# Kernel tuning notes

Measured on AMD Instinct MI355X. Metric: run time of the kernel, lower is better.

The kernel has to match this reference:

```python
import jax, jax.numpy as jnp
import numpy as np
from jax import lax

B, T, I = 256, 720, 16   # batch, seq_len, input_dim
H = 128                  # hidden_dim
PRED_LEN = 96


def lstm_cell(x, h, c, W_ih, W_hh, b):
    # PyTorch gate order: i, f, g, o ; b = b_ih + b_hh (combined)
    gates = x @ W_ih.T + h @ W_hh.T + b
    i, f, g, o = jnp.split(gates, 4, axis=-1)
    c = jax.nn.sigmoid(f) * c + jax.nn.sigmoid(i) * jnp.tanh(g)
    h = jax.nn.sigmoid(o) * jnp.tanh(c)
    return h, c


def setup_inputs() -> dict:
    key = jax.random.key(0)
    ks = jax.random.split(key, 16)
    k = 1.0 / np.sqrt(H)
    u = lambda kk, shape: jax.random.uniform(kk, shape, jnp.float32, -k, k)
    inp = {
        "x": jax.random.normal(ks[0], (B, T, I), jnp.float32),
        # encoder (bidirectional, 1 layer): forward + backward directions
        "e_Wih_f": u(ks[1], (4 * H, I)), "e_Whh_f": u(ks[2], (4 * H, H)), "e_b_f": u(ks[3], (4 * H,)),
        "e_Wih_b": u(ks[4], (4 * H, I)), "e_Whh_b": u(ks[5], (4 * H, H)), "e_b_b": u(ks[6], (4 * H,)),
        # decoder (bidirectional, 1 layer)
        "d_Wih_f": u(ks[7], (4 * H, I)), "d_Whh_f": u(ks[8], (4 * H, H)), "d_b_f": u(ks[9], (4 * H,)),
        "d_Wih_b": u(ks[10], (4 * H, I)), "d_Whh_b": u(ks[11], (4 * H, H)), "d_b_b": u(ks[12], (4 * H,)),
        # final linear: (2H -> I)
        "W_lin": u(ks[13], (I, 2 * H)), "b_lin": u(ks[14], (I,)),
    }
    return inp


def reference(x, e_Wih_f, e_Whh_f, e_b_f, e_Wih_b, e_Whh_b, e_b_b,
              d_Wih_f, d_Whh_f, d_b_f, d_Wih_b, d_Whh_b, d_b_b,
              W_lin, b_lin):
    xt = jnp.transpose(x, (1, 0, 2))  # [T, B, I] time-major
    h0 = jnp.zeros((B, H), x.dtype)
    c0 = jnp.zeros((B, H), x.dtype)

    # ---- encoder: bidirectional LSTM; only final (h, c) per direction is used ----
    def enc_f(carry, xt_t):
        h, c = lstm_cell(xt_t, carry[0], carry[1], e_Wih_f, e_Whh_f, e_b_f)
        return (h, c), None

    def enc_b(carry, xt_t):
        h, c = lstm_cell(xt_t, carry[0], carry[1], e_Wih_b, e_Whh_b, e_b_b)
        return (h, c), None

    (hf, cf), _ = lax.scan(enc_f, (h0, c0), xt)
    (hb, cb), _ = lax.scan(enc_b, (h0, c0), xt[::-1])

    def dec_step(carry, _):
        inp, hf, cf, hb, cb = carry
        hf, cf = lstm_cell(inp, hf, cf, d_Wih_f, d_Whh_f, d_b_f)
        hb, cb = lstm_cell(inp, hb, cb, d_Wih_b, d_Whh_b, d_b_b)
        # seq_len==1 so out_f = forward hidden, out_b = backward hidden
        out = jnp.concatenate([hf, hb], axis=-1) @ W_lin.T + b_lin  # [B, I]
        return (out, hf, cf, hb, cb), out

    init = (x[:, -1, :], hf, cf, hb, cb)
    _, outs = lax.scan(dec_step, init, None, length=PRED_LEN)  # [P, B, I]
    return jnp.transpose(outs, (1, 0, 2))  # [B, pred_len, I]
```

## Files before the change

### kernel.cpp

```cpp
#include <hip/hip_runtime.h>
#include <math.h>

#define TB    720
#define NI    16
#define NH    128
#define NG    512
#define PRED  96
#define CHUNK 90

typedef _Float16 h2    __attribute__((ext_vector_type(2)));
typedef _Float16 f16x4 __attribute__((ext_vector_type(4)));
typedef _Float16 f16x8 __attribute__((ext_vector_type(8)));
typedef float    f32x4 __attribute__((ext_vector_type(4)));

#define LOG2E  1.4426950408889634f
#define LOG2E2 2.8853900817779268f

__device__ __forceinline__ float rcpf_(float v) {
#if __has_builtin(__builtin_amdgcn_rcpf)
    return __builtin_amdgcn_rcpf(v);
#else
    return 1.0f / v;
#endif
}
__device__ __forceinline__ float ex2(float v) {
#if __has_builtin(__builtin_amdgcn_exp2f)
    return __builtin_amdgcn_exp2f(v);
#else
    return exp2f(v);
#endif
}

__device__ __forceinline__ unsigned int packf16(float a, float b) {
    h2 p; p.x = (_Float16)a; p.y = (_Float16)b;
    return __builtin_bit_cast(unsigned int, p);
}
__device__ __forceinline__ f32x4 MFMA(f16x8 a, f16x8 b, f32x4 c) {
    return __builtin_amdgcn_mfma_f32_16x16x32_f16(a, b, c, 0, 0, 0);
}
__device__ __forceinline__ f16x8 mk8s(const float* p, float s) {
    f16x8 v;
    v[0] = (_Float16)(p[0]  * s); v[1] = (_Float16)(p[1]  * s);
    v[2] = (_Float16)(p[2]  * s); v[3] = (_Float16)(p[3]  * s);
    v[4] = (_Float16)(p[16] * s); v[5] = (_Float16)(p[17] * s);
    v[6] = (_Float16)(p[18] * s); v[7] = (_Float16)(p[19] * s);
    return v;
}
__device__ __forceinline__ int opaque(int v) { asm volatile("" : "+v"(v)); return v; }

#define CELLBODY(CV, CS, HWPTR, CWBV) { \
    float ei_ = ex2(-(CV)[0]), ef_ = ex2(-(CV)[1]); \
    float eg_ = ex2((CV)[2]),  eo_ = ex2(-(CV)[3]); \
    float di_ = 1.f + ei_, df_ = 1.f + ef_, dg_ = 1.f + eg_, dq_ = 1.f + eo_; \
    float r1_ = rcpf_(di_ * df_), r2_ = rcpf_(dq_ * dg_); \
    float si_ = r1_ * df_, sf_ = r1_ * di_, so_ = r2_ * dg_; \
    float tg_ = __builtin_fmaf(-2.f * r2_, dq_, 1.f); \
    (CS) = sf_ * (CS) + si_ * tg_; \
    float ec_ = ex2((CS) * LOG2E2); \
    float th_ = __builtin_fmaf(-2.f, rcpf_(1.f + ec_), 1.f); \
    float hv_ = so_ * th_; \
    *(_Float16*)((char*)(HWPTR) + (CWBV)) = (_Float16)hv_; }

__global__ __launch_bounds__(1024, 4)
void enc_kernel(const float* __restrict__ x,
                const float* __restrict__ Wih_f, const float* __restrict__ Whh_f, const float* __restrict__ b_f,
                const float* __restrict__ Wih_b, const float* __restrict__ Whh_b, const float* __restrict__ b_b,
                float* __restrict__ st)
{
    __shared__ _Float16 hbuf0[16 * NH];
    __shared__ _Float16 hbuf1[16 * NH];
    __shared__ unsigned int xsh[CHUNK * 128];

    const int blk = blockIdx.x;
    const int dir = blk & 1;
    const int b0  = (blk >> 1) << 4;
    const int t   = threadIdx.x;
    const int wv  = t >> 6;
    const int l   = t & 63;
    const int lr  = l & 15;
    const int lk  = l >> 4;

    const float* Wih = dir ? Wih_b : Wih_f;
    const float* Whh = dir ? Whh_b : Whh_f;
    const float* bv  = dir ? b_b   : b_f;

    const int mt0 = 2 * wv, mt1 = 2 * wv + 1;
    const int R0 = mt0 * 16 + lr, R1 = mt1 * 16 + lr;
    const int or0 = (R0 & 3) * 128 + (R0 >> 2);
    const int or1 = (R1 & 3) * 128 + (R1 >> 2);
    const float s0 = ((or0 >> 7) == 2) ? LOG2E2 : LOG2E;
    const float s1 = ((or1 >> 7) == 2) ? LOG2E2 : LOG2E;
    const float* p0 = Whh + (size_t)or0 * NH + lk * 4;
    const float* p1 = Whh + (size_t)or1 * NH + lk * 4;
    f16x8 w0_0 = mk8s(p0, s0), w0_1 = mk8s(p0 + 32, s0), w0_2 = mk8s(p0 + 64, s0), w0_3 = mk8s(p0 + 96, s0);
    f16x8 w1_0 = mk8s(p1, s1), w1_1 = mk8s(p1 + 32, s1), w1_2 = mk8s(p1 + 64, s1), w1_3 = mk8s(p1 + 96, s1);

    f16x8 ax0, ax1;
#define MKAXR(DST, OR, SC) { \
    const float* xr_ = Wih + (size_t)(OR) * NI + lk * 4; \
    DST[0] = (_Float16)(xr_[0] * (SC)); DST[1] = (_Float16)(xr_[1] * (SC)); \
    DST[2] = (_Float16)(xr_[2] * (SC)); DST[3] = (_Float16)(xr_[3] * (SC)); \
    DST[4] = (_Float16)(bv[(OR)] * (SC)); \
    DST[5] = (_Float16)0.f; DST[6] = (_Float16)0.f; DST[7] = (_Float16)0.f; }
    MKAXR(ax0, or0, s0) MKAXR(ax1, or1, s1)
#undef MKAXR

    const int d0 = mt0 * 4 + lk, d1 = mt1 * 4 + lk;

    ((unsigned int*)hbuf0)[t] = 0u;
    float cs0 = 0.f, cs1 = 0.f;

    const int hro0 = 0 * 1024 + lk * 256 + lr * 16;
    const int hro1 = 1 * 1024 + lk * 256 + lr * 16;
    const int hro2 = 2 * 1024 + lk * 256 + lr * 16;
    const int hro3 = 3 * 1024 + lk * 256 + lr * 16;
#define CWB(D) ((((D) >> 5) * 1024) + ((((D) & 15) >> 2) * 256) + lr * 16 + (((((D) & 31) >> 4) * 4 + ((D) & 3)) * 2))
    const int cwb0 = CWB(d0), cwb1 = CWB(d1);
#undef CWB
    const int xoff = lk * 128 + lr * 8;
    const unsigned int oneku = (lk == 0) ? 0x00003c00u : 0u;
    const f32x4 CZ = {0.f, 0.f, 0.f, 0.f};
    __syncthreads();

#define STEP(HR, HW, SI) { \
    const char* hrb_ = (const char*)(HR); \
    f16x8 bx; \
    { uint2 xq_ = *(const uint2*)((const char*)xsh + (SI) * 512 + xoff); \
      ((unsigned int*)&bx)[0] = xq_.x; ((unsigned int*)&bx)[1] = xq_.y; \
      ((unsigned int*)&bx)[2] = oneku; ((unsigned int*)&bx)[3] = 0u; } \
    f32x4 C0 = MFMA(ax0, bx, CZ); \
    f32x4 C1 = MFMA(ax1, bx, CZ); \
    f16x8 bh_; \
    bh_ = *(const f16x8*)(hrb_ + hro0); \
    C0 = MFMA(w0_0, bh_, C0); C1 = MFMA(w1_0, bh_, C1); \
    bh_ = *(const f16x8*)(hrb_ + hro1); \
    C0 = MFMA(w0_1, bh_, C0); C1 = MFMA(w1_1, bh_, C1); \
    bh_ = *(const f16x8*)(hrb_ + hro2); \
    C0 = MFMA(w0_2, bh_, C0); C1 = MFMA(w1_2, bh_, C1); \
    bh_ = *(const f16x8*)(hrb_ + hro3); \
    C0 = MFMA(w0_3, bh_, C0); C1 = MFMA(w1_3, bh_, C1); \
    CELLBODY(C0, cs0, HW, cwb0) \
    CELLBODY(C1, cs1, HW, cwb1) \
    __syncthreads(); }

    for (int c = 0; c < 8; ++c) {
        {
            const int c0 = c * CHUNK;
            for (int i = t; i < 16 * CHUNK * 8; i += 1024) {
                const int br  = i / (CHUNK * 8);
                const int rem = i - br * (CHUNK * 8);
                const int ti  = rem >> 3;
                const int dw  = rem & 7;
                const int s_  = c0 + ti;
                const int tt  = dir ? (TB - 1 - s_) : s_;
                float2 v = *(const float2*)(x + ((size_t)(b0 + br) * TB + tt) * NI + dw * 2);
                xsh[ti * 128 + (dw >> 1) * 32 + br * 2 + (dw & 1)] = packf16(v.x, v.y);
            }
        }
        __syncthreads();
        for (int si2 = 0; si2 < CHUNK / 2; ++si2) {
            STEP(hbuf0, hbuf1, si2 * 2)
            STEP(hbuf1, hbuf0, si2 * 2 + 1)
        }
    }
#undef STEP

    {
        const size_t base = ((size_t)(b0 + lr) * 2 + dir) * 2 * NH;
#define CWB(D) ((((D) >> 5) * 1024) + ((((D) & 15) >> 2) * 256) + lr * 16 + (((((D) & 31) >> 4) * 4 + ((D) & 3)) * 2))
        st[base + d0]      = (float)*(const _Float16*)((const char*)hbuf0 + CWB(d0));
        st[base + NH + d0] = cs0;
        st[base + d1]      = (float)*(const _Float16*)((const char*)hbuf0 + CWB(d1));
        st[base + NH + d1] = cs1;
#undef CWB
    }
}

__global__ __launch_bounds__(1024, 4)
void dec_kernel(const float* __restrict__ x,
                const float* __restrict__ Wih_f, const float* __restrict__ Whh_f, const float* __restrict__ b_f,
                const float* __restrict__ Wih_b, const float* __restrict__ Whh_b, const float* __restrict__ b_b,
                const float* __restrict__ Wlin, const float* __restrict__ blin,
                const float* __restrict__ st, float* __restrict__ out)
{
    __shared__ _Float16 hF0[16 * NH], hF1[16 * NH];
    __shared__ _Float16 hB0[16 * NH], hB1[16 * NH];
    __shared__ unsigned int wlin_s[8 * 64 * 4];
    __shared__ unsigned int inpH[16 * 8];
    __shared__ float obuf[PRED * 16 * 16];

    const int b0   = blockIdx.x << 4;
    const int t    = threadIdx.x;
    const int wv   = t >> 6;
    const int cell = wv >> 3;
    const int wvv  = wv & 7;
    const int l    = t & 63;
    const int lr   = l & 15;
    const int lk   = l >> 4;

    const float* Wih = cell ? Wih_b : Wih_f;
    const float* Whh = cell ? Whh_b : Whh_f;
    const float* bv  = cell ? b_b   : b_f;

    if (t < 512) {
        const int f = t >> 6, ll = t & 63;
        const int elr = ll & 15, elk = ll >> 4;
        const float* wr = Wlin + elr * 256 + f * 32 + elk * 4;
        uint4 q;
        q.x = packf16(wr[0],  wr[1]);  q.y = packf16(wr[2],  wr[3]);
        q.z = packf16(wr[16], wr[17]); q.w = packf16(wr[18], wr[19]);
        *(uint4*)&wlin_s[(f * 64 + ll) * 4] = q;
    }

    const int mt0 = 4 * wvv, mt1 = 4 * wvv + 1, mt2 = 4 * wvv + 2, mt3 = 4 * wvv + 3;
    const int R0 = mt0 * 16 + lr, R1 = mt1 * 16 + lr, R2 = mt2 * 16 + lr, R3 = mt3 * 16 + lr;
    const int or0 = (R0 & 3) * 128 + (R0 >> 2);
    const int or1 = (R1 & 3) * 128 + (R1 >> 2);
    const int or2 = (R2 & 3) * 128 + (R2 >> 2);
    const int or3 = (R3 & 3) * 128 + (R3 >> 2);
    const float s0 = ((or0 >> 7) == 2) ? LOG2E2 : LOG2E;
    const float s1 = ((or1 >> 7) == 2) ? LOG2E2 : LOG2E;
    const float s2 = ((or2 >> 7) == 2) ? LOG2E2 : LOG2E;
    const float s3 = ((or3 >> 7) == 2) ? LOG2E2 : LOG2E;
    const float* p0 = Whh + (size_t)or0 * NH + lk * 4;
    const float* p1 = Whh + (size_t)or1 * NH + lk * 4;
    const float* p2 = Whh + (size_t)or2 * NH + lk * 4;
    const float* p3 = Whh + (size_t)or3 * NH + lk * 4;
    f16x8 w0_0 = mk8s(p0, s0), w0_1 = mk8s(p0 + 32, s0), w0_2 = mk8s(p0 + 64, s0), w0_3 = mk8s(p0 + 96, s0);
    f16x8 w1_0 = mk8s(p1, s1), w1_1 = mk8s(p1 + 32, s1), w1_2 = mk8s(p1 + 64, s1), w1_3 = mk8s(p1 + 96, s1);
    f16x8 w2_0 = mk8s(p2, s2), w2_1 = mk8s(p2 + 32, s2), w2_2 = mk8s(p2 + 64, s2), w2_3 = mk8s(p2 + 96, s2);
    f16x8 w3_0 = mk8s(p3, s3), w3_1 = mk8s(p3 + 32, s3), w3_2 = mk8s(p3 + 64, s3), w3_3 = mk8s(p3 + 96, s3);

    f16x8 ax0, ax1, ax2, ax3;
#define MKAXR(DST, OR, SC) { \
    const float* xr_ = Wih + (size_t)(OR) * NI + lk * 4; \
    DST[0] = (_Float16)(xr_[0] * (SC)); DST[1] = (_Float16)(xr_[1] * (SC)); \
    DST[2] = (_Float16)(xr_[2] * (SC)); DST[3] = (_Float16)(xr_[3] * (SC)); \
    DST[4] = (_Float16)(bv[(OR)] * (SC)); \
    DST[5] = (_Float16)0.f; DST[6] = (_Float16)0.f; DST[7] = (_Float16)0.f; }
    MKAXR(ax0, or0, s0) MKAXR(ax1, or1, s1) MKAXR(ax2, or2, s2) MKAXR(ax3, or3, s3)
#undef MKAXR

    const int d0 = mt0 * 4 + lk, d1 = mt1 * 4 + lk, d2 = mt2 * 4 + lk, d3 = mt3 * 4 + lk;

    const int hro0 = 0 * 1024 + lk * 256 + lr * 16;
    const int hro1 = 1 * 1024 + lk * 256 + lr * 16;
    const int hro2 = 2 * 1024 + lk * 256 + lr * 16;
    const int hro3 = 3 * 1024 + lk * 256 + lr * 16;
#define CWB(D) ((((D) >> 5) * 1024) + ((((D) & 15) >> 2) * 256) + lr * 16 + (((((D) & 31) >> 4) * 4 + ((D) & 3)) * 2))
    const int cwb0 = CWB(d0), cwb1 = CWB(d1), cwb2 = CWB(d2), cwb3 = CWB(d3);
    float cs0, cs1, cs2, cs3;
    {
        _Float16* hini = cell ? hB0 : hF0;
        const size_t bs = ((size_t)(b0 + lr) * 2 + cell) * 2 * NH;
        *(_Float16*)((char*)hini + cwb0) = (_Float16)st[bs + d0];  cs0 = st[bs + NH + d0];
        *(_Float16*)((char*)hini + cwb1) = (_Float16)st[bs + d1];  cs1 = st[bs + NH + d1];
        *(_Float16*)((char*)hini + cwb2) = (_Float16)st[bs + d2];  cs2 = st[bs + NH + d2];
        *(_Float16*)((char*)hini + cwb3) = (_Float16)st[bs + d3];  cs3 = st[bs + NH + d3];
    }
#undef CWB
    if (t < 128) {
        const int ilr = t >> 3, idw = t & 7;
        const float2 v = *(const float2*)(x + ((size_t)(b0 + ilr) * TB + (TB - 1)) * NI + idw * 2);
        inpH[ilr * 8 + idw] = packf16(v.x, v.y);
    }
    const float bl0 = blin[4 * lk + 0], bl1 = blin[4 * lk + 1];
    const float bl2 = blin[4 * lk + 2], bl3 = blin[4 * lk + 3];
    const unsigned int oneku = (lk == 0) ? 0x00003c00u : 0u;
    const f32x4 CZ = {0.f, 0.f, 0.f, 0.f};
    __syncthreads();

#define STEPD(HRF, HWF, HRB, HWB, S) { \
    const char* hr_ = cell ? (const char*)(HRB) : (const char*)(HRF); \
    char*       hw_ = cell ? (char*)(HWB)       : (char*)(HWF); \
    f16x8 bx; \
    { uint2 xq_ = *(const uint2*)((const char*)inpH + lr * 32 + lk * 8); \
      ((unsigned int*)&bx)[0] = xq_.x; ((unsigned int*)&bx)[1] = xq_.y; \
      ((unsigned int*)&bx)[2] = oneku; ((unsigned int*)&bx)[3] = 0u; } \
    f32x4 C0 = MFMA(ax0, bx, CZ); f32x4 C1 = MFMA(ax1, bx, CZ); \
    f32x4 C2 = MFMA(ax2, bx, CZ); f32x4 C3 = MFMA(ax3, bx, CZ); \
    f16x8 bh_; \
    bh_ = *(const f16x8*)(hr_ + hro0); \
    C0 = MFMA(w0_0, bh_, C0); C1 = MFMA(w1_0, bh_, C1); \
    C2 = MFMA(w2_0, bh_, C2); C3 = MFMA(w3_0, bh_, C3); \
    bh_ = *(const f16x8*)(hr_ + hro1); \
    C0 = MFMA(w0_1, bh_, C0); C1 = MFMA(w1_1, bh_, C1); \
    C2 = MFMA(w2_1, bh_, C2); C3 = MFMA(w3_1, bh_, C3); \
    bh_ = *(const f16x8*)(hr_ + hro2); \
    C0 = MFMA(w0_2, bh_, C0); C1 = MFMA(w1_2, bh_, C1); \
    C2 = MFMA(w2_2, bh_, C2); C3 = MFMA(w3_2, bh_, C3); \
    bh_ = *(const f16x8*)(hr_ + hro3); \
    C0 = MFMA(w0_3, bh_, C0); C1 = MFMA(w1_3, bh_, C1); \
    C2 = MFMA(w2_3, bh_, C2); C3 = MFMA(w3_3, bh_, C3); \
    CELLBODY(C0, cs0, hw_, cwb0) \
    CELLBODY(C1, cs1, hw_, cwb1) \
    CELLBODY(C2, cs2, hw_, cwb2) \
    CELLBODY(C3, cs3, hw_, cwb3) \
    __syncthreads(); \
    if (wv == 0) { \
        f32x4 P = CZ; \
        f16x8 af_, bf_; \
        _Pragma("unroll") \
        for (int f = 0; f < 8; ++f) { \
            af_ = *(const f16x8*)((const char*)wlin_s + opaque((f * 64 + l) * 16)); \
            const char* hb_ = (f < 4) ? (const char*)(HWF) + f * 1024 \
                                      : (const char*)(HWB) + (f - 4) * 1024; \
            bf_ = *(const f16x8*)(hb_ + lk * 256 + lr * 16); \
            P = MFMA(af_, bf_, P); \
        } \
        float o0 = P[0] + bl0, o1 = P[1] + bl1, o2 = P[2] + bl2, o3 = P[3] + bl3; \
        float* ob_ = obuf + (S) * 256 + (4 * lk) * 16 + lr; \
        ob_[0] = o0; ob_[16] = o1; ob_[32] = o2; ob_[48] = o3; \
        inpH[lr * 8 + lk * 2]     = packf16(o0, o1); \
        inpH[lr * 8 + lk * 2 + 1] = packf16(o2, o3); \
    } \
    __syncthreads(); }

    for (int s2 = 0; s2 < PRED / 2; ++s2) {
        STEPD(hF0, hF1, hB0, hB1, s2 * 2)
        STEPD(hF1, hF0, hB1, hB0, s2 * 2 + 1)
    }
#undef STEPD

    for (int i = t; i < PRED * 256; i += 1024) {
        const int lr2 = i / (PRED * NI);
        const int rem = i - lr2 * (PRED * NI);
        const int s   = rem >> 4;
        const int j   = rem & 15;
        out[(size_t)(b0 + lr2) * PRED * NI + rem] = obuf[s * 256 + j * 16 + lr2];
    }
}

extern "C" void kernel_launch(void* const* d_in, const int* in_sizes, int n_in,
                              void* d_out, int out_size, void* d_ws, size_t ws_size,
                              hipStream_t stream)
{
    const float* x      = (const float*)d_in[0];
    const float* eWih_f = (const float*)d_in[1];
    const float* eWhh_f = (const float*)d_in[2];
    const float* eb_f   = (const float*)d_in[3];
    const float* eWih_b = (const float*)d_in[4];
    const float* eWhh_b = (const float*)d_in[5];
    const float* eb_b   = (const float*)d_in[6];
    const float* dWih_f = (const float*)d_in[7];
    const float* dWhh_f = (const float*)d_in[8];
    const float* db_f   = (const float*)d_in[9];
    const float* dWih_b = (const float*)d_in[10];
    const float* dWhh_b = (const float*)d_in[11];
    const float* db_b   = (const float*)d_in[12];
    const float* Wlin   = (const float*)d_in[13];
    const float* blin   = (const float*)d_in[14];

    float* st = (float*)d_ws;

    enc_kernel<<<32, 1024, 0, stream>>>(x, eWih_f, eWhh_f, eb_f, eWih_b, eWhh_b, eb_b, st);
    dec_kernel<<<16, 1024, 0, stream>>>(x, dWih_f, dWhh_f, db_f, dWih_b, dWhh_b, db_b,
                                        Wlin, blin, st, (float*)d_out);
}
```

Measured before the change: 734.6 us.

## Overlap decoder recurrent h-matmul with output projection in the same barrier phase

Splits each decoder step so the recurrent W_hh·h MFMAs for the next step are issued right after the cell update, in the same barrier phase where wave 0 computes the linear output projection. Only the small input-projection MFMAs stay on the critical path after the projected input is available. This shortens the serial dependency chain per autoregressive step. In exchange it keeps extra accumulator registers live across the barrier and adds a prologue h-matmul.

```diff
diff --git a/kernel.cpp b/kernel.cpp
--- a/kernel.cpp
+++ b/kernel.cpp
@@ -270,57 +270,71 @@
     const f32x4 CZ = {0.f, 0.f, 0.f, 0.f};
     __syncthreads();
 
-#define STEPD(HRF, HWF, HRB, HWB, S) { \
+    f32x4 Ch0, Ch1, Ch2, Ch3;
+
+#define CHCOMP(HRF, HRB) { \
     const char* hr_ = cell ? (const char*)(HRB) : (const char*)(HRF); \
-    char*       hw_ = cell ? (char*)(HWB)       : (char*)(HWF); \
+    f16x8 bh_; \
+    bh_ = *(const f16x8*)(hr_ + hro0); \
+    Ch0 = MFMA(w0_0, bh_, CZ);  Ch1 = MFMA(w1_0, bh_, CZ); \
+    Ch2 = MFMA(w2_0, bh_, CZ);  Ch3 = MFMA(w3_0, bh_, CZ); \
+    bh_ = *(const f16x8*)(hr_ + hro1); \
+    Ch0 = MFMA(w0_1, bh_, Ch0); Ch1 = MFMA(w1_1, bh_, Ch1); \
+    Ch2 = MFMA(w2_1, bh_, Ch2); Ch3 = MFMA(w3_1, bh_, Ch3); \
+    bh_ = *(const f16x8*)(hr_ + hro2); \
+    Ch0 = MFMA(w0_2, bh_, Ch0); Ch1 = MFMA(w1_2, bh_, Ch1); \
+    Ch2 = MFMA(w2_2, bh_, Ch2); Ch3 = MFMA(w3_2, bh_, Ch3); \
+    bh_ = *(const f16x8*)(hr_ + hro3); \
+    Ch0 = MFMA(w0_3, bh_, Ch0); Ch1 = MFMA(w1_3, bh_, Ch1); \
+    Ch2 = MFMA(w2_3, bh_, Ch2); Ch3 = MFMA(w3_3, bh_, Ch3); }
+
+#define P3BODY(HRF, HRB, S) { \
+    f32x4 P = CZ; \
+    _Pragma("unroll") \
+    for (int f = 0; f < 8; ++f) { \
+        f16x8 af_ = *(const f16x8*)((const char*)wlin_s + opaque((f * 64 + l) * 16)); \
+        const char* hb_ = (f < 4) ? (const char*)(HRF) + f * 1024 \
+                                  : (const char*)(HRB) + (f - 4) * 1024; \
+        f16x8 bf_ = *(const f16x8*)(hb_ + lk * 256 + lr * 16); \
+        P = MFMA(af_, bf_, P); \
+    } \
+    float o0 = P[0] + bl0, o1 = P[1] + bl1, o2 = P[2] + bl2, o3 = P[3] + bl3; \
+    float* ob_ = obuf + (S) * 256 + (4 * lk) * 16 + lr; \
+    ob_[0] = o0; ob_[16] = o1; ob_[32] = o2; ob_[48] = o3; \
+    inpH[lr * 8 + lk * 2]     = packf16(o0, o1); \
+    inpH[lr * 8 + lk * 2 + 1] = packf16(o2, o3); }
+
+#define STEPA(HWF, HWB) { \
+    char* hw_ = cell ? (char*)(HWB) : (char*)(HWF); \
     f16x8 bx; \
     { uint2 xq_ = *(const uint2*)((const char*)inpH + lr * 32 + lk * 8); \
       ((unsigned int*)&bx)[0] = xq_.x; ((unsigned int*)&bx)[1] = xq_.y; \
       ((unsigned int*)&bx)[2] = oneku; ((unsigned int*)&bx)[3] = 0u; } \
-    f32x4 C0 = MFMA(ax0, bx, CZ); f32x4 C1 = MFMA(ax1, bx, CZ); \
-    f32x4 C2 = MFMA(ax2, bx, CZ); f32x4 C3 = MFMA(ax3, bx, CZ); \
-    f16x8 bh_; \
-    bh_ = *(const f16x8*)(hr_ + hro0); \
-    C0 = MFMA(w0_0, bh_, C0); C1 = MFMA(w1_0, bh_, C1); \
-    C2 = MFMA(w2_0, bh_, C2); C3 = MFMA(w3_0, bh_, C3); \
-    bh_ = *(const f16x8*)(hr_ + hro1); \
-    C0 = MFMA(w0_1, bh_, C0); C1 = MFMA(w1_1, bh_, C1); \
-    C2 = MFMA(w2_1, bh_, C2); C3 = MFMA(w3_1, bh_, C3); \
-    bh_ = *(const f16x8*)(hr_ + hro2); \
-    C0 = MFMA(w0_2, bh_, C0); C1 = MFMA(w1_2, bh_, C1); \
-    C2 = MFMA(w2_2, bh_, C2); C3 = MFMA(w3_2, bh_, C3); \
-    bh_ = *(const f16x8*)(hr_ + hro3); \
-    C0 = MFMA(w0_3, bh_, C0); C1 = MFMA(w1_3, bh_, C1); \
-    C2 = MFMA(w2_3, bh_, C2); C3 = MFMA(w3_3, bh_, C3); \
+    f32x4 C0 = MFMA(ax0, bx, Ch0); f32x4 C1 = MFMA(ax1, bx, Ch1); \
+    f32x4 C2 = MFMA(ax2, bx, Ch2); f32x4 C3 = MFMA(ax3, bx, Ch3); \
     CELLBODY(C0, cs0, hw_, cwb0) \
     CELLBODY(C1, cs1, hw_, cwb1) \
     CELLBODY(C2, cs2, hw_, cwb2) \
     CELLBODY(C3, cs3, hw_, cwb3) \
-    __syncthreads(); \
-    if (wv == 0) { \
-        f32x4 P = CZ; \
-        f16x8 af_, bf_; \
-        _Pragma("unroll") \
-        for (int f = 0; f < 8; ++f) { \
-            af_ = *(const f16x8*)((const char*)wlin_s + opaque((f * 64 + l) * 16)); \
-            const char* hb_ = (f < 4) ? (const char*)(HWF) + f * 1024 \
-                                      : (const char*)(HWB) + (f - 4) * 1024; \
-            bf_ = *(const f16x8*)(hb_ + lk * 256 + lr * 16); \
-            P = MFMA(af_, bf_, P); \
-        } \
-        float o0 = P[0] + bl0, o1 = P[1] + bl1, o2 = P[2] + bl2, o3 = P[3] + bl3; \
-        float* ob_ = obuf + (S) * 256 + (4 * lk) * 16 + lr; \
-        ob_[0] = o0; ob_[16] = o1; ob_[32] = o2; ob_[48] = o3; \
-        inpH[lr * 8 + lk * 2]     = packf16(o0, o1); \
-        inpH[lr * 8 + lk * 2 + 1] = packf16(o2, o3); \
-    } \
     __syncthreads(); }
 
+#define STEPB(HRF, HRB, S) { \
+    CHCOMP(HRF, HRB) \
+    if (wv == 0) { P3BODY(HRF, HRB, S) } \
+    __syncthreads(); }
+
+    CHCOMP(hF0, hB0)
+
     for (int s2 = 0; s2 < PRED / 2; ++s2) {
-        STEPD(hF0, hF1, hB0, hB1, s2 * 2)
-        STEPD(hF1, hF0, hB1, hB0, s2 * 2 + 1)
-    }
-#undef STEPD
+        STEPA(hF1, hB1)
+        STEPB(hF1, hB1, s2 * 2)
+        STEPA(hF0, hB0)
+        STEPB(hF0, hB0, s2 * 2 + 1)
+    }
+#undef STEPB
+#undef STEPA
+#undef P3BODY
+#undef CHCOMP
 
     for (int i = t; i < PRED * 256; i += 1024) {
         const int lr2 = i / (PRED * NI);
```

Result: slower. 797.6 us (+8.6%).
